# Performance work log

Hardware: AMD Instinct MI355X
Metric: run time of the kernel (lower is better)

## Reference

```python
import jax, jax.numpy as jnp
import numpy as np

B, T, V, C = 64, 256, 256, 4
NEG = -jnp.inf


def setup_inputs() -> dict:
    key = jax.random.key(0)
    k1, k2, k3 = jax.random.split(key, 3)
    logits = jax.random.normal(k1, (B, T, V, C), dtype=jnp.float32)
    ar_sent = jax.random.randint(k2, (B, T), 0, 61, dtype=jnp.int32)
    en_sent = jax.random.randint(k3, (B, V), 0, 61, dtype=jnp.int32)
    return {"logits": logits, "ar_sent": ar_sent, "en_sent": en_sent}


def _forward_alpha(ins, dele, sub):
    # ins/dele/sub: [B,T,V] log-scores of insertion/deletion/substitution into cell (t,v)
    b, t_len, v_len = ins.shape
    z = jnp.zeros((b, 1), ins.dtype)
    # row t=0: only insertions -> prefix sum
    alpha0 = jnp.concatenate([z, jnp.cumsum(ins[:, 0, 1:], axis=1)], axis=1)

    def step(prev, xs):
        ins_t, del_t, sub_t = xs  # each [B,V]
        # c[v]: contributions from previous row (deletion + substitution)
        c = jnp.concatenate(
            [del_t[:, :1] + prev[:, :1],
             jnp.logaddexp(del_t[:, 1:] + prev[:, 1:], sub_t[:, 1:] + prev[:, :-1])],
            axis=1)
        # within-row recurrence alpha[v] = logaddexp(ins[v]+alpha[v-1], c[v])
        # solved in closed form: alpha[v] = S[v] + logcumsumexp_k<=v (c[k]-S[k]), S=prefix sum of ins
        s = jnp.concatenate([z, jnp.cumsum(ins_t[:, 1:], axis=1)], axis=1)
        row = s + jax.lax.cumlogsumexp(c - s, axis=1)
        return row, row

    xs = (jnp.moveaxis(ins, 1, 0)[1:], jnp.moveaxis(dele, 1, 0)[1:], jnp.moveaxis(sub, 1, 0)[1:])
    _, rows = jax.lax.scan(step, alpha0, xs)
    return jnp.moveaxis(jnp.concatenate([alpha0[None], rows], axis=0), 0, 1)  # [B,T,V]


def _backward_beta(ins, dele, sub):
    b, t_len, v_len = ins.shape
    z = jnp.zeros((b, 1), ins.dtype)
    # row t=T-1: only insertions -> suffix sum, corner = 0
    ins_last = ins[:, -1, :]
    beta_last = jnp.concatenate([jnp.cumsum(ins_last[:, -2::-1], axis=1)[:, ::-1], z], axis=1)

    def step(nxt, xs):
        ins_t, del_t, sub_t = xs
        # c[v]: contributions from next row (deletion + substitution); v=V-1 has no substitution
        c = jnp.concatenate(
            [jnp.logaddexp(del_t[:, :-1] + nxt[:, :-1], sub_t[:, :-1] + nxt[:, 1:]),
             del_t[:, -1:] + nxt[:, -1:]],
            axis=1)
        # beta[v] = logaddexp(ins[v]+beta[v+1], c[v]): reverse linear recurrence -> flip + closed form
        fins = ins_t[:, ::-1]
        fc = c[:, ::-1]
        fs = jnp.concatenate([z, jnp.cumsum(fins[:, 1:], axis=1)], axis=1)
        fb = fs + jax.lax.cumlogsumexp(fc - fs, axis=1)
        row = fb[:, ::-1]
        return row, row

    xs = (jnp.moveaxis(ins, 1, 0)[:-1][::-1],
          jnp.moveaxis(dele, 1, 0)[:-1][::-1],
          jnp.moveaxis(sub, 1, 0)[:-1][::-1])
    _, rows = jax.lax.scan(step, beta_last, xs)
    beta = jnp.concatenate([rows[::-1], beta_last[None]], axis=0)
    return jnp.moveaxis(beta, 0, 1)  # [B,T,V]


def reference(logits, ar_sent, en_sent):
    # tiny_table class ids: deletion=0, insertion=1, substitution=2 (constant, char-independent)
    scores = jax.nn.log_softmax(logits, axis=3)  # [B,T,V,4]
    dele, ins, sub = scores[..., 0], scores[..., 1], scores[..., 2]
    alpha = _forward_alpha(ins, dele, sub)

    # beta / expected counts are computed under no_grad in the original
    sg = jax.lax.stop_gradient
    s = sg(scores)
    a = sg(alpha)
    beta = _backward_beta(s[..., 1], s[..., 0], s[..., 2])

    bsz, t_len, v_len, n_cls = scores.shape
    cls = jnp.arange(n_cls)[None, None, :]
    t_lt = (jnp.arange(t_len) < t_len - 1)[:, None, None]
    v_lt = (jnp.arange(v_len) < v_len - 1)[None, :, None]
    pd = jnp.broadcast_to(jnp.where((cls == 0) & t_lt, 0.0, NEG), (t_len, v_len, n_cls))
    pi = jnp.broadcast_to(jnp.where((cls == 1) & v_lt, 0.0, NEG), (t_len, v_len, n_cls))
    ps = jnp.broadcast_to(jnp.where((cls == 2) & t_lt & v_lt, 0.0, NEG), (t_len, v_len, n_cls))

    full = jnp.full((bsz, t_len, v_len, n_cls), NEG, scores.dtype)
    ed = full.at[:, 1:].set(a[:, :-1, :, None] + s[:, 1:] + pd[None, 1:] + beta[:, 1:, :, None])
    ei = full.at[:, :, 1:].set(a[:, :, :-1, None] + s[:, :, 1:] + pi[None, :, 1:] + beta[:, :, 1:, None])
    es = full.at[:, 1:, 1:].set(
        a[:, :-1, :-1, None] + s[:, 1:, 1:] + ps[None, 1:, 1:] + beta[:, 1:, 1:, None])

    ec = jnp.logaddexp(jnp.logaddexp(ed, ei), es)
    norm = jax.nn.logsumexp(ec, axis=3, keepdims=True)
    norm = jnp.where(jnp.isneginf(norm), 0.0, norm)  # avoid nan at degenerate (0,0)-type cells
    expected_counts = jnp.exp(ec - norm)
    return (scores, expected_counts, alpha[0, -1, -1])
```

## Files before the change

kernel.cpp:

```cpp
#include <hip/hip_runtime.h>
#include <math.h>

#define BB 64
#define TT 256
#define VV 256
#define SLABS 321
#define SLAB_F (SLABS * 256)
#define PLANE ((size_t)BB * SLAB_F)
#define EPLANE ((size_t)BB * SLABS * 64)
#define NSLAB_W 319

typedef __attribute__((ext_vector_type(4))) _Float16 half4;

__device__ __forceinline__ float dpp_shr1_f(float x) {
    return __int_as_float(__builtin_amdgcn_update_dpp(
        __float_as_int(x), __float_as_int(x), 0x138, 0xF, 0xF, false));
}
__device__ __forceinline__ int dpp_shr1_i(int x) {
    return __builtin_amdgcn_update_dpp(x, x, 0x138, 0xF, 0xF, false);
}

__device__ __forceinline__ float lae2(float x, float y) {
    float m = fmaxf(x, y);
    float d = x - y;
    return m + __logf(1.0f + __expf(-fabsf(d)));
}

__global__ void __launch_bounds__(256) k_prep(const float4* __restrict__ lg,
                                              float4* __restrict__ sc,
                                              _Float16* __restrict__ Dd,
                                              _Float16* __restrict__ Di,
                                              _Float16* __restrict__ Du) {
    int blk = blockIdx.x;
    int b = blk / NSLAB_W;
    int s = blk - b * NSLAB_W;
    int v = threadIdx.x;
    int t = s - (v >> 2);
    bool valid = (t >= 0) && (t < TT);
    int tc = valid ? t : 0;
    size_t ci = ((size_t)b << 16) | ((size_t)tc << 8) | (size_t)v;
    float4 x = lg[ci];
    float m = fmaxf(fmaxf(x.x, x.y), fmaxf(x.z, x.w));
    float e0 = __expf(x.x - m), e1 = __expf(x.y - m);
    float e2 = __expf(x.z - m), e3 = __expf(x.w - m);
    float ssum = e0 + e1 + e2 + e3;
    float l = m + __logf(ssum);
    if (valid) sc[ci] = make_float4(x.x - l, x.y - l, x.z - l, x.w - l);
    float rcp = valid ? (1.0f / ssum) : 0.0f;
    size_t pb = (size_t)b * SLAB_F + ((size_t)s << 8) + v;
    Dd[pb] = (_Float16)(e0 * rcp);
    Di[pb] = (_Float16)(e1 * rcp);
    Du[pb] = (_Float16)(e2 * rcp);
}

__global__ void __launch_bounds__(64) k_dp(const _Float16* __restrict__ Pd,
                                           const _Float16* __restrict__ Pi,
                                           const _Float16* __restrict__ Pu,
                                           float* __restrict__ A,
                                           int* __restrict__ Ei,
                                           float* __restrict__ scalar_out) {
    const int b = blockIdx.x;
    const int lane = threadIdx.x;
    const bool l0 = (lane == 0);
    const size_t base = (size_t)b * SLAB_F + (lane << 2);

    const half4* __restrict__ pd = (const half4*)(Pd + base);
    const half4* __restrict__ pi = (const half4*)(Pi + base);
    const half4* __restrict__ pu = (const half4*)(Pu + base);
    float4* __restrict__ pa = (float4*)(A + base);
    int* __restrict__ pe = Ei + (size_t)b * SLABS * 64 + lane;
    const int SS = 64;

    half4 d0,d1,d2,d3,d4,d5,d6,d7;
    half4 i0,i1,i2,i3,i4,i5,i6,i7;
    half4 u0,u1,u2,u3,u4,u5,u6,u7;
    d0 = pd[0*SS]; i0 = pi[0*SS]; u0 = pu[0*SS];
    d1 = pd[1*SS]; i1 = pi[1*SS]; u1 = pu[1*SS];
    d2 = pd[2*SS]; i2 = pi[2*SS]; u2 = pu[2*SS];
    d3 = pd[3*SS]; i3 = pi[3*SS]; u3 = pu[3*SS];
    d4 = pd[4*SS]; i4 = pi[4*SS]; u4 = pu[4*SS];
    d5 = pd[5*SS]; i5 = pi[5*SS]; u5 = pu[5*SS];
    d6 = pd[6*SS]; i6 = pi[6*SS]; u6 = pu[6*SS];
    d7 = pd[7*SS]; i7 = pi[7*SS]; u7 = pu[7*SS];

    float A0 = 0.0f, A1 = 0.0f, A2 = 0.0f, A3 = 0.0f;
    int   E  = 0;
    float LC = 0.0f, LP = 0.0f;
    int   EC = 0,    EP = 0;
    float sA3 = 0.0f;
    int   sEn = 0;

    int s = 0;

#define STEP(DD, II, UU, FIXUP, CLAMP, CAP)                                       \
    {                                                                             \
        const half4 dl = DD, in = II, su = UU;                                    \
        {                                                                         \
            int sp = s + 8;                                                       \
            if (CLAMP) sp = sp > SLABS - 1 ? SLABS - 1 : sp;                      \
            DD = pd[sp * SS]; II = pi[sp * SS]; UU = pu[sp * SS];                 \
        }                                                                         \
        int E_eff = E;                                                            \
        bool isT0 = false;                                                        \
        if (FIXUP) {                                                              \
            isT0 = (s == lane);                                                   \
            E_eff = isT0 ? (l0 ? 0 : EC) : E;                                     \
        }                                                                         \
        const float lc = l0 ? 0.0f : ldexpf(LC, EC - E_eff);                      \
        const float lp = l0 ? 0.0f : ldexpf(LP, EP - E_eff);                      \
        float X0 = (float)dl.x * A0 + (float)su.x * lp;                           \
        float X1 = (float)dl.y * A1 + (float)su.y * A0;                           \
        float X2 = (float)dl.z * A2 + (float)su.z * A1;                           \
        float X3 = (float)dl.w * A3 + (float)su.w * A2;                           \
        if (FIXUP && isT0) {                                                      \
            X0 = l0 ? 1.0f : 0.0f; X1 = 0.0f; X2 = 0.0f; X3 = 0.0f;               \
        }                                                                         \
        const float iy = (float)in.y, iz = (float)in.z, iw = (float)in.w;         \
        const float B0 = X0;                                                      \
        const float B1 = fmaf(B0, iy, X1);                                        \
        const float B2 = fmaf(B1, iz, X2);                                        \
        const float B3 = fmaf(B2, iw, X3);                                        \
        const float Q0 = (float)in.x;                                             \
        const float Q1 = Q0 * iy;                                                 \
        const float Q2 = Q1 * iz;                                                 \
        const float Q3 = Q2 * iw;                                                 \
        float nA0 = fmaf(lc, Q0, B0);                                             \
        float nA1 = fmaf(lc, Q1, B1);                                             \
        float nA2 = fmaf(lc, Q2, B2);                                             \
        float nA3 = fmaf(lc, Q3, B3);                                             \
        const int eb = (int)((__float_as_uint(nA3) >> 23) & 255u) - 126;          \
        const int En = E_eff + eb;                                                \
        nA3 = ldexpf(nA3, -eb);                                                   \
        nA0 = ldexpf(nA0, -eb);                                                   \
        nA1 = ldexpf(nA1, -eb);                                                   \
        nA2 = ldexpf(nA2, -eb);                                                   \
        LP = LC; EP = EC;                                                         \
        LC = dpp_shr1_f(nA3);                                                     \
        EC = dpp_shr1_i(En);                                                      \
        pa[s * SS] = make_float4(nA0, nA1, nA2, nA3);                             \
        pe[s * 64] = En;                                                          \
        if (CAP && s == TT + 62) { sA3 = nA3; sEn = En; }     \
        A0 = nA0; A1 = nA1; A2 = nA2; A3 = nA3; E = En;                           \
        ++s;                                                                      \
    }

#pragma unroll 1
    for (int it = 0; it < 8; ++it) {
        STEP(d0, i0, u0, 1, 0, 0);
        STEP(d1, i1, u1, 1, 0, 0);
        STEP(d2, i2, u2, 1, 0, 0);
        STEP(d3, i3, u3, 1, 0, 0);
        STEP(d4, i4, u4, 1, 0, 0);
        STEP(d5, i5, u5, 1, 0, 0);
        STEP(d6, i6, u6, 1, 0, 0);
        STEP(d7, i7, u7, 1, 0, 0);
    }
#pragma unroll 1
    for (int it = 0; it < 31; ++it) {
        STEP(d0, i0, u0, 0, 0, 0);
        STEP(d1, i1, u1, 0, 0, 0);
        STEP(d2, i2, u2, 0, 0, 0);
        STEP(d3, i3, u3, 0, 0, 0);
        STEP(d4, i4, u4, 0, 0, 0);
        STEP(d5, i5, u5, 0, 0, 0);
        STEP(d6, i6, u6, 0, 0, 0);
        STEP(d7, i7, u7, 0, 0, 0);
    }
    STEP(d0, i0, u0, 0, 1, 1);
    STEP(d1, i1, u1, 0, 1, 1);
    STEP(d2, i2, u2, 0, 1, 1);
    STEP(d3, i3, u3, 0, 1, 1);
    STEP(d4, i4, u4, 0, 1, 1);
    STEP(d5, i5, u5, 0, 1, 1);
    STEP(d6, i6, u6, 0, 1, 1);
    STEP(d7, i7, u7, 0, 1, 1);
#undef STEP

    if ((b == 0) && (lane == 63))
        scalar_out[0] = logf(sA3) + (float)sEn * 0.6931471805599453f;
}

__global__ void __launch_bounds__(256) k_counts(const _Float16* __restrict__ Pd,
                                                const _Float16* __restrict__ Pi,
                                                const _Float16* __restrict__ Pu,
                                                const float* __restrict__ A,
                                                const int* __restrict__ Ei,
                                                float4* __restrict__ out) {
    int blk = blockIdx.x;
    int b = blk / NSLAB_W;
    int s = blk - b * NSLAB_W;
    int v = threadIdx.x;
    int g = v >> 2;
    int t = s - g;
    if ((t < 0) | (t >= TT)) return;

    size_t ab = (size_t)b * SLAB_F;
    size_t ebp = (size_t)b * SLABS * 64;
    int sm1 = s > 0 ? s - 1 : 0;
    int sm2 = s > 1 ? s - 2 : 0;
    int vm = v ? v - 1 : 0;
    int gm = g ? g - 1 : 0;
    bool v4 = (v & 3) == 0;

    float pD = (float)Pd[ab + ((size_t)s << 8) + v];
    float pI = (float)Pi[ab + ((size_t)s << 8) + v];
    float pU = (float)Pu[ab + ((size_t)s << 8) + v];
    float AA = A[ab + ((size_t)s   << 8) + v];
    float AU = A[ab + ((size_t)sm1 << 8) + v];
    int   EA = Ei[ebp + s   * 64 + g];
    int   EU = Ei[ebp + sm1 * 64 + g];
    float AL = v4 ? A[ab + ((size_t)sm1 << 8) + vm] : A[ab + ((size_t)s   << 8) + vm];
    int   EL = v4 ? Ei[ebp + sm1 * 64 + gm] : EA;
    float AD = v4 ? A[ab + ((size_t)sm2 << 8) + vm] : A[ab + ((size_t)sm1 << 8) + vm];
    int   ED = v4 ? Ei[ebp + sm2 * 64 + gm] : EU;

    bool tE = (t == 0) | (t == TT - 1);
    bool vE = (v == 0) | (v == VV - 1);
    float inv = 1.0f / AA;
    float w0 = ldexpf(pD * AU * inv, EU - EA);
    float w1 = ldexpf(pI * AL * inv, EL - EA);
    float w2 = ldexpf(pU * AD * inv, ED - EA);
    float4 o;
    o.x = tE ? 0.0f : (vE ? 1.0f : w0);
    o.y = vE ? 0.0f : (tE ? 1.0f : w1);
    o.z = (tE | vE) ? 0.0f : w2;
    o.w = 0.0f;
    out[((size_t)b << 16) | ((size_t)t << 8) | (size_t)v] = o;
}

__global__ void k_prep_legacy(const float4* __restrict__ lg, float4* __restrict__ sc, int n) {
    int i = blockIdx.x * blockDim.x + threadIdx.x;
    int st = gridDim.x * blockDim.x;
    for (; i < n; i += st) {
        float4 x = lg[i];
        float m = fmaxf(fmaxf(x.x, x.y), fmaxf(x.z, x.w));
        float s = __expf(x.x - m) + __expf(x.y - m) + __expf(x.z - m) + __expf(x.w - m);
        float l = m + __logf(s);
        sc[i] = make_float4(x.x - l, x.y - l, x.z - l, x.w - l);
    }
}
__global__ void __launch_bounds__(64) k_dp_legacy(const float4* __restrict__ scores,
                                                  float4* __restrict__ counts,
                                                  float* __restrict__ scalar_out) {
    const int b = blockIdx.x;
    const int lane = threadIdx.x;
    const int v0 = lane << 2;
    const float4* __restrict__ srow = scores + ((size_t)b * TT * VV + v0);
    float4* __restrict__ crow = counts + ((size_t)b * TT * VV + v0);
    float4 P0[4], P1[4], P2[4];
    {
        int r; const float4* p;
        r = 0 - lane; r = r < 0 ? 0 : r; p = srow + (size_t)r * VV;
        P0[0]=p[0]; P0[1]=p[1]; P0[2]=p[2]; P0[3]=p[3];
        r = 1 - lane; r = r < 0 ? 0 : r; p = srow + (size_t)r * VV;
        P1[0]=p[0]; P1[1]=p[1]; P1[2]=p[2]; P1[3]=p[3];
        r = 2 - lane; r = r < 0 ? 0 : r; p = srow + (size_t)r * VV;
        P2[0]=p[0]; P2[1]=p[1]; P2[2]=p[2]; P2[3]=p[3];
    }
    float aPrev[4] = { -INFINITY, -INFINITY, -INFINITY, -INFINITY };
    float leftPrev = -INFINITY, leftCur = -INFINITY;
    int s = 0;
#define STEPL(BUF)                                                                \
    {                                                                             \
        const int t = s - lane;                                                   \
        const bool active = (t >= 0) && (t < TT);                                 \
        float4 c0 = BUF[0], c1 = BUF[1], c2 = BUF[2], c3 = BUF[3];                \
        {                                                                         \
            int tp = t + 3; tp = tp < 0 ? 0 : tp; tp = tp > TT - 1 ? TT - 1 : tp; \
            const float4* lp = srow + (size_t)tp * VV;                            \
            BUF[0]=lp[0]; BUF[1]=lp[1]; BUF[2]=lp[2]; BUF[3]=lp[3];               \
        }                                                                         \
        float aPm1_0 = (lane == 0) ? -INFINITY : leftPrev;                        \
        float cv0 = lae2(c0.x + aPrev[0], c0.z + aPm1_0);                         \
        float cv1 = lae2(c1.x + aPrev[1], c1.z + aPrev[0]);                       \
        float cv2 = lae2(c2.x + aPrev[2], c2.z + aPrev[1]);                       \
        float cv3 = lae2(c3.x + aPrev[3], c3.z + aPrev[2]);                       \
        if (lane == 0) cv0 = c0.x + aPrev[0];                                     \
        if (t == 0) {                                                             \
            cv0 = (lane == 0) ? 0.0f : -INFINITY;                                 \
            cv1 = -INFINITY; cv2 = -INFINITY; cv3 = -INFINITY;                    \
        }                                                                         \
        float lc = (lane == 0) ? -INFINITY : leftCur;                             \
        float a0 = lae2(lc + c0.y, cv0);                                          \
        float a1 = lae2(a0 + c1.y, cv1);                                          \
        float a2 = lae2(a1 + c2.y, cv2);                                          \
        float a3 = lae2(a2 + c3.y, cv3);                                          \
        if (active) {                                                             \
            const bool tE = (t == 0) | (t == TT - 1);                             \
            float aCm1[4] = { lc, a0, a1, a2 };                                   \
            float aPm1[4] = { aPm1_0, aPrev[0], aPrev[1], aPrev[2] };             \
            float aP[4]   = { aPrev[0], aPrev[1], aPrev[2], aPrev[3] };           \
            float aA[4]   = { a0, a1, a2, a3 };                                   \
            float4 sv[4]  = { c0, c1, c2, c3 };                                   \
            float4* cp = crow + (size_t)t * VV;                                   \
            _Pragma("unroll")                                                     \
            for (int k = 0; k < 4; ++k) {                                         \
                const bool vE = (k == 0 && lane == 0) || (k == 3 && lane == 63);  \
                float w0 = __expf(aP[k]   + sv[k].x - aA[k]);                     \
                float w1 = __expf(aCm1[k] + sv[k].y - aA[k]);                     \
                float w2 = __expf(aPm1[k] + sv[k].z - aA[k]);                     \
                float4 o;                                                         \
                o.x = tE ? 0.0f : (vE ? 1.0f : w0);                               \
                o.y = vE ? 0.0f : (tE ? 1.0f : w1);                               \
                o.z = (tE || vE) ? 0.0f : w2;                                     \
                o.w = 0.0f;                                                       \
                cp[k] = o;                                                        \
            }                                                                     \
            if ((t == TT - 1) && (lane == 63) && (b == 0)) scalar_out[0] = a3;    \
        }                                                                         \
        aPrev[0]=a0; aPrev[1]=a1; aPrev[2]=a2; aPrev[3]=a3;                       \
        leftPrev = leftCur;                                                       \
        leftCur = __shfl_up(a3, 1);                                               \
        ++s;                                                                      \
    }
#pragma unroll 1
    for (int it = 0; it < 107; ++it) { STEPL(P0); STEPL(P1); STEPL(P2); }
#undef STEPL
}

extern "C" void kernel_launch(void* const* d_in, const int* in_sizes, int n_in,
                              void* d_out, int out_size, void* d_ws, size_t ws_size,
                              hipStream_t stream) {
    const float* logits = (const float*)d_in[0];
    float* out = (float*)d_out;
    const size_t ncell = (size_t)BB * TT * VV;

    float4* scores = (float4*)out;
    float4* counts = (float4*)(out + ncell * 4);
    float* scalar_out = out + ncell * 8;

    _Float16* Pd = (_Float16*)d_ws;
    _Float16* Pi = Pd + PLANE;
    _Float16* Pu = Pi + PLANE;
    float* Aa = (float*)(Pu + PLANE);
    int*   Ee = (int*)(Aa + PLANE);

    size_t need = PLANE * 2 * 3 + PLANE * 4 + EPLANE * 4;
    if (ws_size >= need) {
        k_prep<<<BB * NSLAB_W, 256, 0, stream>>>((const float4*)logits, scores, Pd, Pi, Pu);
        k_dp<<<BB, 64, 0, stream>>>(Pd, Pi, Pu, Aa, Ee, scalar_out);
        k_counts<<<BB * NSLAB_W, 256, 0, stream>>>(Pd, Pi, Pu, Aa, Ee, counts);
    } else {
        k_prep_legacy<<<2048, 256, 0, stream>>>((const float4*)logits, scores, (int)ncell);
        k_dp_legacy<<<BB, 64, 0, stream>>>(scores, counts, scalar_out);
    }
}
```

Measured before the change: 106.9 us.

## Compute posterior weights inside DP sweep and store them as fp16

```diff
diff --git a/kernel.cpp b/kernel.cpp
--- a/kernel.cpp
+++ b/kernel.cpp
@@ -7,7 +7,6 @@
 #define SLABS 321
 #define SLAB_F (SLABS * 256)
 #define PLANE ((size_t)BB * SLAB_F)
-#define EPLANE ((size_t)BB * SLABS * 64)
 #define NSLAB_W 319
 
 typedef __attribute__((ext_vector_type(4))) _Float16 half4;
@@ -56,8 +55,8 @@
 __global__ void __launch_bounds__(64) k_dp(const _Float16* __restrict__ Pd,
                                            const _Float16* __restrict__ Pi,
                                            const _Float16* __restrict__ Pu,
-                                           float* __restrict__ A,
-                                           int* __restrict__ Ei,
+                                           _Float16* __restrict__ W0,
+                                           _Float16* __restrict__ W1,
                                            float* __restrict__ scalar_out) {
     const int b = blockIdx.x;
     const int lane = threadIdx.x;
@@ -67,8 +66,8 @@
     const half4* __restrict__ pd = (const half4*)(Pd + base);
     const half4* __restrict__ pi = (const half4*)(Pi + base);
     const half4* __restrict__ pu = (const half4*)(Pu + base);
-    float4* __restrict__ pa = (float4*)(A + base);
-    int* __restrict__ pe = Ei + (size_t)b * SLABS * 64 + lane;
+    half4* __restrict__ pw0 = (half4*)(W0 + base);
+    half4* __restrict__ pw1 = (half4*)(W1 + base);
     const int SS = 64;
 
     half4 d0,d1,d2,d3,d4,d5,d6,d7;
@@ -128,6 +127,22 @@
         float nA1 = fmaf(lc, Q1, B1);                                             \
         float nA2 = fmaf(lc, Q2, B2);                                             \
         float nA3 = fmaf(lc, Q3, B3);                                             \
+                           \
+        const float r0 = __builtin_amdgcn_rcpf(nA0);                              \
+        const float r1 = __builtin_amdgcn_rcpf(nA1);                              \
+        const float r2 = __builtin_amdgcn_rcpf(nA2);                              \
+        const float r3 = __builtin_amdgcn_rcpf(nA3);                              \
+        half4 h0, h1;                                                             \
+        h0.x = (_Float16)((float)dl.x * A0 * r0);                                 \
+        h0.y = (_Float16)((float)dl.y * A1 * r1);                                 \
+        h0.z = (_Float16)((float)dl.z * A2 * r2);                                 \
+        h0.w = (_Float16)((float)dl.w * A3 * r3);                                 \
+        h1.x = (_Float16)(Q0 * lc * r0);                                          \
+        h1.y = (_Float16)(iy * nA0 * r1);                                         \
+        h1.z = (_Float16)(iz * nA1 * r2);                                         \
+        h1.w = (_Float16)(iw * nA2 * r3);                                         \
+        pw0[s * SS] = h0;                                                         \
+        pw1[s * SS] = h1;                                                         \
         const int eb = (int)((__float_as_uint(nA3) >> 23) & 255u) - 126;          \
         const int En = E_eff + eb;                                                \
         nA3 = ldexpf(nA3, -eb);                                                   \
@@ -137,8 +152,6 @@
         LP = LC; EP = EC;                                                         \
         LC = dpp_shr1_f(nA3);                                                     \
         EC = dpp_shr1_i(En);                                                      \
-        pa[s * SS] = make_float4(nA0, nA1, nA2, nA3);                             \
-        pe[s * 64] = En;                                                          \
         if (CAP && s == TT + 62) { sA3 = nA3; sEn = En; }     \
         A0 = nA0; A1 = nA1; A2 = nA2; A3 = nA3; E = En;                           \
         ++s;                                                                      \
@@ -180,12 +193,9 @@
         scalar_out[0] = logf(sA3) + (float)sEn * 0.6931471805599453f;
 }
 
-__global__ void __launch_bounds__(256) k_counts(const _Float16* __restrict__ Pd,
-                                                const _Float16* __restrict__ Pi,
-                                                const _Float16* __restrict__ Pu,
-                                                const float* __restrict__ A,
-                                                const int* __restrict__ Ei,
-                                                float4* __restrict__ out) {
+__global__ void __launch_bounds__(256) k_wperm(const _Float16* __restrict__ W0,
+                                               const _Float16* __restrict__ W1,
+                                               float4* __restrict__ out) {
     int blk = blockIdx.x;
     int b = blk / NSLAB_W;
     int s = blk - b * NSLAB_W;
@@ -194,32 +204,15 @@
     int t = s - g;
     if ((t < 0) | (t >= TT)) return;
 
-    size_t ab = (size_t)b * SLAB_F;
-    size_t ebp = (size_t)b * SLABS * 64;
-    int sm1 = s > 0 ? s - 1 : 0;
-    int sm2 = s > 1 ? s - 2 : 0;
-    int vm = v ? v - 1 : 0;
-    int gm = g ? g - 1 : 0;
-    bool v4 = (v & 3) == 0;
-
-    float pD = (float)Pd[ab + ((size_t)s << 8) + v];
-    float pI = (float)Pi[ab + ((size_t)s << 8) + v];
-    float pU = (float)Pu[ab + ((size_t)s << 8) + v];
-    float AA = A[ab + ((size_t)s   << 8) + v];
-    float AU = A[ab + ((size_t)sm1 << 8) + v];
-    int   EA = Ei[ebp + s   * 64 + g];
-    int   EU = Ei[ebp + sm1 * 64 + g];
-    float AL = v4 ? A[ab + ((size_t)sm1 << 8) + vm] : A[ab + ((size_t)s   << 8) + vm];
-    int   EL = v4 ? Ei[ebp + sm1 * 64 + gm] : EA;
-    float AD = v4 ? A[ab + ((size_t)sm2 << 8) + vm] : A[ab + ((size_t)sm1 << 8) + vm];
-    int   ED = v4 ? Ei[ebp + sm2 * 64 + gm] : EU;
+    size_t pb = (size_t)b * SLAB_F + ((size_t)s << 8) + v;
+    float w0 = (float)W0[pb];
+    float w1 = (float)W1[pb];
+    w0 = fminf(fmaxf(w0, 0.0f), 1.0f);
+    w1 = fminf(fmaxf(w1, 0.0f), 1.0f);
+    float w2 = fmaxf(0.0f, 1.0f - w0 - w1);
 
     bool tE = (t == 0) | (t == TT - 1);
     bool vE = (v == 0) | (v == VV - 1);
-    float inv = 1.0f / AA;
-    float w0 = ldexpf(pD * AU * inv, EU - EA);
-    float w1 = ldexpf(pI * AL * inv, EL - EA);
-    float w2 = ldexpf(pU * AD * inv, ED - EA);
     float4 o;
     o.x = tE ? 0.0f : (vE ? 1.0f : w0);
     o.y = vE ? 0.0f : (tE ? 1.0f : w1);
@@ -332,14 +325,14 @@
     _Float16* Pd = (_Float16*)d_ws;
     _Float16* Pi = Pd + PLANE;
     _Float16* Pu = Pi + PLANE;
-    float* Aa = (float*)(Pu + PLANE);
-    int*   Ee = (int*)(Aa + PLANE);
-
-    size_t need = PLANE * 2 * 3 + PLANE * 4 + EPLANE * 4;
+    _Float16* W0 = Pu + PLANE;
+    _Float16* W1 = W0 + PLANE;
+
+    size_t need = PLANE * 2 * 5;
     if (ws_size >= need) {
         k_prep<<<BB * NSLAB_W, 256, 0, stream>>>((const float4*)logits, scores, Pd, Pi, Pu);
-        k_dp<<<BB, 64, 0, stream>>>(Pd, Pi, Pu, Aa, Ee, scalar_out);
-        k_counts<<<BB * NSLAB_W, 256, 0, stream>>>(Pd, Pi, Pu, Aa, Ee, counts);
+        k_dp<<<BB, 64, 0, stream>>>(Pd, Pi, Pu, W0, W1, scalar_out);
+        k_wperm<<<BB * NSLAB_W, 256, 0, stream>>>(W0, W1, counts);
     } else {
         k_prep_legacy<<<2048, 256, 0, stream>>>((const float4*)logits, scores, (int)ncell);
         k_dp_legacy<<<BB, 64, 0, stream>>>(scores, counts, scalar_out);
```

After: 105.3 us. Within noise of the previous version (-1.5%).
